# Optimization experiments

Hardware: AMD Instinct MI355X
Metric: run time of the kernel (lower is better)

Reference implementation:

```python
import jax, jax.numpy as jnp
import numpy as np
from jax.scipy.special import logsumexp

N_ITERS = 20


def setup_inputs() -> dict:
    key = jax.random.key(0)
    k1, _ = jax.random.split(key)
    cost_matrix = jax.random.uniform(k1, (64, 1024, 1024), dtype=jnp.float32)
    epsilon = jnp.ones((1,), dtype=jnp.float32)
    return {"cost_matrix": cost_matrix, "epsilon": epsilon}


def reference(cost_matrix, epsilon):
    # log-space Sinkhorn: alternate row / column normalization in log domain
    log_alpha = -cost_matrix / epsilon  # (B, N, N)

    def step(la, _):
        la = la - logsumexp(la, axis=-1, keepdims=True)  # row normalize
        la = la - logsumexp(la, axis=-2, keepdims=True)  # col normalize
        return la, None

    log_alpha, _ = jax.lax.scan(step, log_alpha, None, length=N_ITERS)
    return jnp.exp(log_alpha)
```

## Files before the change

kernel.cpp:

```cpp
#include <hip/hip_runtime.h>
#include <hip/hip_fp16.h>


#define BATCH 64
#define N 1024
#define NITERS 20
#define RPB 64
#define BPB 16
#define NBLK (BATCH * BPB)
#define THREADS 256
#define NU2 (N / 4)
#define NU4 (N / 8)
#define NU4F8 (N / 16)
#define NGRP 64
#define BAR_WORDS 128
#define PART_ELEMS ((size_t)2 * BATCH * BPB * N)
#define CSUM_FB_ELEMS ((size_t)NITERS * BATCH * N)

typedef float f32x2 __attribute__((ext_vector_type(2)));

union H2U { __half2 h; unsigned u; };

__device__ __forceinline__ float4 h4_to_f4(uint2 r) {
    H2U a, b;
    a.u = r.x; b.u = r.y;
    float2 fa = __half22float2(a.h);
    float2 fb = __half22float2(b.h);
    return make_float4(fa.x, fa.y, fb.x, fb.y);
}

__device__ __forceinline__ void h8_unpack(uint4 r, float* f) {
    H2U a, b, c, d;
    a.u = r.x; b.u = r.y; c.u = r.z; d.u = r.w;
    float2 fa = __half22float2(a.h), fb = __half22float2(b.h);
    float2 fc = __half22float2(c.h), fd = __half22float2(d.h);
    f[0] = fa.x; f[1] = fa.y; f[2] = fb.x; f[3] = fb.y;
    f[4] = fc.x; f[5] = fc.y; f[6] = fd.x; f[7] = fd.y;
}

__device__ __forceinline__ uint4 h8_pack(const float* f) {
    H2U a, b, c, d;
    a.h = __float22half2_rn(make_float2(f[0], f[1]));
    b.h = __float22half2_rn(make_float2(f[2], f[3]));
    c.h = __float22half2_rn(make_float2(f[4], f[5]));
    d.h = __float22half2_rn(make_float2(f[6], f[7]));
    uint4 r; r.x = a.u; r.y = b.u; r.z = c.u; r.w = d.u;
    return r;
}

__device__ __forceinline__ uint4 pack_fp8_16(const float* k) {
    uint4 r;
    int a;
    a = __builtin_amdgcn_cvt_pk_fp8_f32(k[0],  k[1],  0, false);
    a = __builtin_amdgcn_cvt_pk_fp8_f32(k[2],  k[3],  a, true);
    r.x = (unsigned)a;
    a = __builtin_amdgcn_cvt_pk_fp8_f32(k[4],  k[5],  0, false);
    a = __builtin_amdgcn_cvt_pk_fp8_f32(k[6],  k[7],  a, true);
    r.y = (unsigned)a;
    a = __builtin_amdgcn_cvt_pk_fp8_f32(k[8],  k[9],  0, false);
    a = __builtin_amdgcn_cvt_pk_fp8_f32(k[10], k[11], a, true);
    r.z = (unsigned)a;
    a = __builtin_amdgcn_cvt_pk_fp8_f32(k[12], k[13], 0, false);
    a = __builtin_amdgcn_cvt_pk_fp8_f32(k[14], k[15], a, true);
    r.w = (unsigned)a;
    return r;
}

__device__ __forceinline__ void unpack_fp8_16(uint4 r, float* f) {
    f32x2 p;
    p = __builtin_amdgcn_cvt_pk_f32_fp8((int)r.x, false); f[0]  = p.x; f[1]  = p.y;
    p = __builtin_amdgcn_cvt_pk_f32_fp8((int)r.x, true);  f[2]  = p.x; f[3]  = p.y;
    p = __builtin_amdgcn_cvt_pk_f32_fp8((int)r.y, false); f[4]  = p.x; f[5]  = p.y;
    p = __builtin_amdgcn_cvt_pk_f32_fp8((int)r.y, true);  f[6]  = p.x; f[7]  = p.y;
    p = __builtin_amdgcn_cvt_pk_f32_fp8((int)r.z, false); f[8]  = p.x; f[9]  = p.y;
    p = __builtin_amdgcn_cvt_pk_f32_fp8((int)r.z, true);  f[10] = p.x; f[11] = p.y;
    p = __builtin_amdgcn_cvt_pk_f32_fp8((int)r.w, false); f[12] = p.x; f[13] = p.y;
    p = __builtin_amdgcn_cvt_pk_f32_fp8((int)r.w, true);  f[14] = p.x; f[15] = p.y;
}

__device__ __forceinline__ float cload(const float* p) {
    return __hip_atomic_load((float*)p, __ATOMIC_RELAXED, __HIP_MEMORY_SCOPE_AGENT);
}
__device__ __forceinline__ void cstore(float* p, float v) {
    __hip_atomic_store(p, v, __ATOMIC_RELAXED, __HIP_MEMORY_SCOPE_AGENT);
}

__global__ __launch_bounds__(THREADS) void sk_zero(float* __restrict__ buf,
                                                   int total) {
    const int i = blockIdx.x * THREADS + threadIdx.x;
    if (i < total) buf[i] = 0.0f;
}

__device__ __forceinline__ void gbar(unsigned* __restrict__ bar,
                                     unsigned& gencount) {
    __syncthreads();
    if (threadIdx.x == 0) {
        asm volatile("" ::: "memory");
        unsigned* grp    = bar;
        unsigned* master = bar + NGRP;
        unsigned* gen    = bar + NGRP + 1;
        const unsigned gid = blockIdx.x & (NGRP - 1);
        if (__hip_atomic_fetch_add(&grp[gid], 1u, __ATOMIC_RELAXED,
                                   __HIP_MEMORY_SCOPE_AGENT) == (NBLK / NGRP) - 1u) {
            if (__hip_atomic_fetch_add(master, 1u, __ATOMIC_RELAXED,
                                       __HIP_MEMORY_SCOPE_AGENT) == NGRP - 1u) {
                #pragma unroll
                for (int i = 0; i < NGRP; ++i)
                    __hip_atomic_store(&grp[i], 0u, __ATOMIC_RELAXED,
                                       __HIP_MEMORY_SCOPE_AGENT);
                __hip_atomic_store(master, 0u, __ATOMIC_RELAXED,
                                   __HIP_MEMORY_SCOPE_AGENT);
                asm volatile("s_waitcnt vmcnt(0)" ::: "memory");
                __hip_atomic_fetch_add(gen, 1u, __ATOMIC_RELAXED,
                                       __HIP_MEMORY_SCOPE_AGENT);
            }
        }
        while (__hip_atomic_load(gen, __ATOMIC_RELAXED,
                                 __HIP_MEMORY_SCOPE_AGENT) == gencount)
            __builtin_amdgcn_s_sleep(2);
        asm volatile("" ::: "memory");
    }
    __syncthreads();
    ++gencount;
}

__global__ __launch_bounds__(THREADS, 4) void sk_fused(
        const float* __restrict__ C, const float* __restrict__ eps,
        uint4* __restrict__ K16, uint4* __restrict__ K8,
        float* __restrict__ part, unsigned* __restrict__ bar,
        float* __restrict__ out) {
    __shared__ float4 smc[4][N / 4];
    __shared__ float vsh[N];
    __shared__ float u_lds[RPB];
    const int t = threadIdx.x;
    const int lane = t & 63, w = t >> 6;
    const int bid = blockIdx.x;
    const int b = bid >> 4, bx = bid & 15;
    const int row0 = bx * RPB + w * 16;
    unsigned gencount = 0;

    {
        const float nie = -1.0f / eps[0];
        const float4* __restrict__ Cp =
            (const float4*)(C + ((size_t)b * N + row0) * N) + lane * 4;
        uint4* __restrict__ Kp16 = K16 + ((size_t)b * N + row0) * NU4 + lane * 2;
        uint4* __restrict__ Kp8  = K8  + ((size_t)b * N + row0) * NU4F8 + lane;

        float colacc[16];
        #pragma unroll
        for (int q = 0; q < 16; ++q) colacc[q] = 0.0f;

        float4 cur[4];
        #pragma unroll
        for (int q = 0; q < 4; ++q) cur[q] = Cp[q];

        #pragma unroll
        for (int i = 0; i < 16; ++i) {
            float4 nxt[4];
            if (i < 15) {
                #pragma unroll
                for (int q = 0; q < 4; ++q) nxt[q] = Cp[(i + 1) * (N / 4) + q];
            }
            float k[16];
            const float* cf = (const float*)cur;
            #pragma unroll
            for (int q = 0; q < 16; ++q) k[q] = __expf(cf[q] * nie);

            Kp16[(size_t)i * NU4]     = h8_pack(k);
            Kp16[(size_t)i * NU4 + 1] = h8_pack(k + 8);
            Kp8[(size_t)i * NU4F8]    = pack_fp8_16(k);

            float s = (((k[0] + k[1]) + (k[2] + k[3])) + ((k[4] + k[5]) + (k[6] + k[7])))
                    + (((k[8] + k[9]) + (k[10] + k[11])) + ((k[12] + k[13]) + (k[14] + k[15])));
            #pragma unroll
            for (int off = 32; off; off >>= 1) s += __shfl_xor(s, off, 64);
            const float ui = 1.0f / s;

            #pragma unroll
            for (int q = 0; q < 16; ++q) colacc[q] += k[q] * ui;

            if (i < 15) {
                #pragma unroll
                for (int q = 0; q < 4; ++q) cur[q] = nxt[q];
            }
        }

        #pragma unroll
        for (int q = 0; q < 4; ++q)
            smc[w][lane * 4 + q] = make_float4(colacc[4 * q], colacc[4 * q + 1],
                                               colacc[4 * q + 2], colacc[4 * q + 3]);
        __syncthreads();
        float4 s0 = smc[0][t], s1 = smc[1][t], s2 = smc[2][t], s3 = smc[3][t];
        float* pw = part + (((size_t)0 * BATCH + b) * BPB + bx) * N + 4 * t;
        cstore(pw + 0, (s0.x + s1.x) + (s2.x + s3.x));
        cstore(pw + 1, (s0.y + s1.y) + (s2.y + s3.y));
        cstore(pw + 2, (s0.z + s1.z) + (s2.z + s3.z));
        cstore(pw + 3, (s0.w + s1.w) + (s2.w + s3.w));
    }
    gbar(bar, gencount);

    const uint4* __restrict__ Kp8r = K8 + ((size_t)b * N + row0) * NU4F8 + lane;
    #pragma unroll 1
    for (int p = 1; p <= 18; ++p) {
        {
            const float* pb =
                part + (((size_t)((p - 1) & 1) * BATCH + b) * BPB) * N + 4 * t;
            float a0 = 0.f, a1 = 0.f, a2 = 0.f, a3 = 0.f;
            #pragma unroll
            for (int j = 0; j < BPB; ++j) {
                const float* pj = pb + (size_t)j * N;
                a0 += cload(pj + 0);
                a1 += cload(pj + 1);
                a2 += cload(pj + 2);
                a3 += cload(pj + 3);
            }
            vsh[4 * t + 0] = 1.0f / a0;
            vsh[4 * t + 1] = 1.0f / a1;
            vsh[4 * t + 2] = 1.0f / a2;
            vsh[4 * t + 3] = 1.0f / a3;
        }
        __syncthreads();
        float vv[16];
        #pragma unroll
        for (int e = 0; e < 16; ++e) vv[e] = vsh[lane * 16 + e];

        float colacc[16];
        #pragma unroll
        for (int q = 0; q < 16; ++q) colacc[q] = 0.0f;

        uint4 buf[4];
        #pragma unroll
        for (int q = 0; q < 4; ++q) buf[q] = Kp8r[(size_t)q * NU4F8];

        #pragma unroll
        for (int i = 0; i < 16; ++i) {
            uint4 nx;
            if (i < 12) nx = Kp8r[(size_t)(i + 4) * NU4F8];

            float k[16];
            unpack_fp8_16(buf[i & 3], k);

            float pa = (k[0] * vv[0] + k[1] * vv[1]) + (k[2] * vv[2] + k[3] * vv[3]);
            float pb = (k[4] * vv[4] + k[5] * vv[5]) + (k[6] * vv[6] + k[7] * vv[7]);
            float pc = (k[8] * vv[8] + k[9] * vv[9]) + (k[10] * vv[10] + k[11] * vv[11]);
            float pd = (k[12] * vv[12] + k[13] * vv[13]) + (k[14] * vv[14] + k[15] * vv[15]);
            float s = (pa + pb) + (pc + pd);

            #pragma unroll
            for (int off = 32; off; off >>= 1) s += __shfl_xor(s, off, 64);
            const float ui = 1.0f / s;

            #pragma unroll
            for (int q = 0; q < 16; ++q) colacc[q] += k[q] * ui;

            if (i < 12) buf[i & 3] = nx;
        }

        #pragma unroll
        for (int q = 0; q < 4; ++q)
            smc[w][lane * 4 + q] = make_float4(colacc[4 * q], colacc[4 * q + 1],
                                               colacc[4 * q + 2], colacc[4 * q + 3]);
        __syncthreads();
        float4 s0 = smc[0][t], s1 = smc[1][t], s2 = smc[2][t], s3 = smc[3][t];
        float* pw = part + (((size_t)(p & 1) * BATCH + b) * BPB + bx) * N + 4 * t;
        cstore(pw + 0, (s0.x + s1.x) + (s2.x + s3.x));
        cstore(pw + 1, (s0.y + s1.y) + (s2.y + s3.y));
        cstore(pw + 2, (s0.z + s1.z) + (s2.z + s3.z));
        cstore(pw + 3, (s0.w + s1.w) + (s2.w + s3.w));
        gbar(bar, gencount);
    }

    {
        {
            const float* pb = part + (((size_t)0 * BATCH + b) * BPB) * N + 4 * t;
            float a0 = 0.f, a1 = 0.f, a2 = 0.f, a3 = 0.f;
            #pragma unroll
            for (int j = 0; j < BPB; ++j) {
                const float* pj = pb + (size_t)j * N;
                a0 += cload(pj + 0);
                a1 += cload(pj + 1);
                a2 += cload(pj + 2);
                a3 += cload(pj + 3);
            }
            vsh[4 * t + 0] = 1.0f / a0;
            vsh[4 * t + 1] = 1.0f / a1;
            vsh[4 * t + 2] = 1.0f / a2;
            vsh[4 * t + 3] = 1.0f / a3;
        }
        __syncthreads();
        float vv[16];
        #pragma unroll
        for (int e = 0; e < 16; ++e) vv[e] = vsh[lane * 16 + e];

        const uint4* __restrict__ Kp = K16 + ((size_t)b * N + row0) * NU4 + lane * 2;

        float colacc[16];
        #pragma unroll
        for (int q = 0; q < 16; ++q) colacc[q] = 0.0f;

        uint4 c0 = Kp[0], c1 = Kp[1];
        #pragma unroll
        for (int i = 0; i < 16; ++i) {
            uint4 n0, n1;
            if (i < 15) {
                n0 = Kp[(size_t)(i + 1) * NU4];
                n1 = Kp[(size_t)(i + 1) * NU4 + 1];
            }
            float k[16];
            h8_unpack(c0, k);
            h8_unpack(c1, k + 8);

            float pa = (k[0] * vv[0] + k[1] * vv[1]) + (k[2] * vv[2] + k[3] * vv[3]);
            float pb = (k[4] * vv[4] + k[5] * vv[5]) + (k[6] * vv[6] + k[7] * vv[7]);
            float pc = (k[8] * vv[8] + k[9] * vv[9]) + (k[10] * vv[10] + k[11] * vv[11]);
            float pd = (k[12] * vv[12] + k[13] * vv[13]) + (k[14] * vv[14] + k[15] * vv[15]);
            float s = (pa + pb) + (pc + pd);

            #pragma unroll
            for (int off = 32; off; off >>= 1) s += __shfl_xor(s, off, 64);
            const float ui = 1.0f / s;
            if (lane == 0) u_lds[w * 16 + i] = ui;

            #pragma unroll
            for (int q = 0; q < 16; ++q) colacc[q] += k[q] * ui;

            if (i < 15) { c0 = n0; c1 = n1; }
        }

        #pragma unroll
        for (int q = 0; q < 4; ++q)
            smc[w][lane * 4 + q] = make_float4(colacc[4 * q], colacc[4 * q + 1],
                                               colacc[4 * q + 2], colacc[4 * q + 3]);
        __syncthreads();
        float4 s0 = smc[0][t], s1 = smc[1][t], s2 = smc[2][t], s3 = smc[3][t];
        float* pw = part + (((size_t)1 * BATCH + b) * BPB + bx) * N + 4 * t;
        cstore(pw + 0, (s0.x + s1.x) + (s2.x + s3.x));
        cstore(pw + 1, (s0.y + s1.y) + (s2.y + s3.y));
        cstore(pw + 2, (s0.z + s1.z) + (s2.z + s3.z));
        cstore(pw + 3, (s0.w + s1.w) + (s2.w + s3.w));
    }
    gbar(bar, gencount);

    {
        {
            const float* pb = part + (((size_t)1 * BATCH + b) * BPB) * N + 4 * t;
            float a0 = 0.f, a1 = 0.f, a2 = 0.f, a3 = 0.f;
            #pragma unroll
            for (int j = 0; j < BPB; ++j) {
                const float* pj = pb + (size_t)j * N;
                a0 += cload(pj + 0);
                a1 += cload(pj + 1);
                a2 += cload(pj + 2);
                a3 += cload(pj + 3);
            }
            vsh[4 * t + 0] = 1.0f / a0;
            vsh[4 * t + 1] = 1.0f / a1;
            vsh[4 * t + 2] = 1.0f / a2;
            vsh[4 * t + 3] = 1.0f / a3;
        }
        __syncthreads();
        const float4 vvf = make_float4(vsh[4 * t + 0], vsh[4 * t + 1],
                                       vsh[4 * t + 2], vsh[4 * t + 3]);
        const size_t rowbase = (size_t)b * N + (size_t)bx * RPB;
        const uint2* __restrict__ K2 = (const uint2*)K16;

        uint2 kc = K2[rowbase * NU2 + t];
        for (int r = 0; r < RPB; ++r) {
            uint2 kn;
            if (r < RPB - 1) kn = K2[(rowbase + r + 1) * NU2 + t];
            const float ur = u_lds[r];
            float4 k = h4_to_f4(kc);
            float4 o;
            o.x = k.x * ur * vvf.x;
            o.y = k.y * ur * vvf.y;
            o.z = k.z * ur * vvf.z;
            o.w = k.w * ur * vvf.w;
            ((float4*)(out + (rowbase + r) * N))[t] = o;
            kc = kn;
        }
    }
}


__global__ __launch_bounds__(THREADS) void sk_build(
        const float* __restrict__ C, const float* __restrict__ eps,
        uint4* __restrict__ K16, uint4* __restrict__ K8,
        float* __restrict__ u, float* __restrict__ csum_out) {
    __shared__ float4 smc[4][N / 4];
    const int t = threadIdx.x;
    const int lane = t & 63, w = t >> 6;
    const int b = blockIdx.y;
    const int row0 = blockIdx.x * RPB + w * 16;
    const float nie = -1.0f / eps[0];

    const float4* __restrict__ Cp =
        (const float4*)(C + ((size_t)b * N + row0) * N) + lane * 4;
    uint4* __restrict__ Kp16 = K16 + ((size_t)b * N + row0) * NU4 + lane * 2;
    uint4* __restrict__ Kp8  = K8  + ((size_t)b * N + row0) * NU4F8 + lane;

    float colacc[16];
    #pragma unroll
    for (int q = 0; q < 16; ++q) colacc[q] = 0.0f;

    float4 cur[4];
    #pragma unroll
    for (int q = 0; q < 4; ++q) cur[q] = Cp[q];

    for (int i = 0; i < 16; ++i) {
        float4 nxt[4];
        if (i < 15) {
            #pragma unroll
            for (int q = 0; q < 4; ++q) nxt[q] = Cp[(i + 1) * (N / 4) + q];
        }
        float k[16];
        const float* cf = (const float*)cur;
        #pragma unroll
        for (int q = 0; q < 16; ++q) k[q] = __expf(cf[q] * nie);

        Kp16[(size_t)i * NU4]     = h8_pack(k);
        Kp16[(size_t)i * NU4 + 1] = h8_pack(k + 8);
        Kp8[(size_t)i * NU4F8]    = pack_fp8_16(k);

        float s = (((k[0] + k[1]) + (k[2] + k[3])) + ((k[4] + k[5]) + (k[6] + k[7])))
                + (((k[8] + k[9]) + (k[10] + k[11])) + ((k[12] + k[13]) + (k[14] + k[15])));
        #pragma unroll
        for (int off = 32; off; off >>= 1) s += __shfl_xor(s, off, 64);
        const float ui = 1.0f / s;
        if (lane == 0) u[b * N + row0 + i] = ui;

        #pragma unroll
        for (int q = 0; q < 16; ++q) colacc[q] += k[q] * ui;

        if (i < 15) {
            #pragma unroll
            for (int q = 0; q < 4; ++q) cur[q] = nxt[q];
        }
    }

    #pragma unroll
    for (int q = 0; q < 4; ++q)
        smc[w][lane * 4 + q] = make_float4(colacc[4 * q], colacc[4 * q + 1],
                                           colacc[4 * q + 2], colacc[4 * q + 3]);
    __syncthreads();
    float4 s0 = smc[0][t], s1 = smc[1][t], s2 = smc[2][t], s3 = smc[3][t];
    float* cs = csum_out + b * N + 4 * t;
    atomicAdd(cs + 0, (s0.x + s1.x) + (s2.x + s3.x));
    atomicAdd(cs + 1, (s0.y + s1.y) + (s2.y + s3.y));
    atomicAdd(cs + 2, (s0.z + s1.z) + (s2.z + s3.z));
    atomicAdd(cs + 3, (s0.w + s1.w) + (s2.w + s3.w));
}

__global__ __launch_bounds__(THREADS) void sk_iter8(
        const uint4* __restrict__ K8, const float* __restrict__ csum_in,
        float* __restrict__ csum_out) {
    __shared__ float4 smc[4][N / 4];
    const int t = threadIdx.x;
    const int lane = t & 63, w = t >> 6;
    const int b = blockIdx.y;
    const int row0 = blockIdx.x * RPB + w * 16;

    const float4* __restrict__ cin = (const float4*)(csum_in + b * N) + lane * 4;
    float vv[16];
    #pragma unroll
    for (int q = 0; q < 4; ++q) {
        float4 c = cin[q];
        vv[4 * q + 0] = 1.0f / c.x;
        vv[4 * q + 1] = 1.0f / c.y;
        vv[4 * q + 2] = 1.0f / c.z;
        vv[4 * q + 3] = 1.0f / c.w;
    }

    const uint4* __restrict__ Kp = K8 + ((size_t)b * N + row0) * NU4F8 + lane;

    float colacc[16];
    #pragma unroll
    for (int q = 0; q < 16; ++q) colacc[q] = 0.0f;

    uint4 c0 = Kp[0];
    uint4 c1 = Kp[NU4F8];
    for (int i = 0; i < 16; ++i) {
        uint4 c2;
        if (i < 14) c2 = Kp[(size_t)(i + 2) * NU4F8];

        float k[16];
        unpack_fp8_16(c0, k);

        float pa = (k[0] * vv[0] + k[1] * vv[1]) + (k[2] * vv[2] + k[3] * vv[3]);
        float pb = (k[4] * vv[4] + k[5] * vv[5]) + (k[6] * vv[6] + k[7] * vv[7]);
        float pc = (k[8] * vv[8] + k[9] * vv[9]) + (k[10] * vv[10] + k[11] * vv[11]);
        float pd = (k[12] * vv[12] + k[13] * vv[13]) + (k[14] * vv[14] + k[15] * vv[15]);
        float s = (pa + pb) + (pc + pd);

        #pragma unroll
        for (int off = 32; off; off >>= 1) s += __shfl_xor(s, off, 64);
        const float ui = 1.0f / s;

        #pragma unroll
        for (int q = 0; q < 16; ++q) colacc[q] += k[q] * ui;

        c0 = c1;
        if (i < 14) c1 = c2;
    }

    #pragma unroll
    for (int q = 0; q < 4; ++q)
        smc[w][lane * 4 + q] = make_float4(colacc[4 * q], colacc[4 * q + 1],
                                           colacc[4 * q + 2], colacc[4 * q + 3]);
    __syncthreads();
    float4 s0 = smc[0][t], s1 = smc[1][t], s2 = smc[2][t], s3 = smc[3][t];
    float* cs = csum_out + b * N + 4 * t;
    atomicAdd(cs + 0, (s0.x + s1.x) + (s2.x + s3.x));
    atomicAdd(cs + 1, (s0.y + s1.y) + (s2.y + s3.y));
    atomicAdd(cs + 2, (s0.z + s1.z) + (s2.z + s3.z));
    atomicAdd(cs + 3, (s0.w + s1.w) + (s2.w + s3.w));
}

__global__ __launch_bounds__(THREADS) void sk_iter(
        const uint4* __restrict__ K, const float* __restrict__ csum_in,
        float* __restrict__ u, float* __restrict__ csum_out) {
    __shared__ float4 smc[4][N / 4];
    const int t = threadIdx.x;
    const int lane = t & 63, w = t >> 6;
    const int b = blockIdx.y;
    const int row0 = blockIdx.x * RPB + w * 16;

    const float4* __restrict__ cin = (const float4*)(csum_in + b * N) + lane * 4;
    float vv[16];
    #pragma unroll
    for (int q = 0; q < 4; ++q) {
        float4 c = cin[q];
        vv[4 * q + 0] = 1.0f / c.x;
        vv[4 * q + 1] = 1.0f / c.y;
        vv[4 * q + 2] = 1.0f / c.z;
        vv[4 * q + 3] = 1.0f / c.w;
    }

    const uint4* __restrict__ Kp = K + ((size_t)b * N + row0) * NU4 + lane * 2;

    float colacc[16];
    #pragma unroll
    for (int q = 0; q < 16; ++q) colacc[q] = 0.0f;

    uint4 c0 = Kp[0], c1 = Kp[1];
    for (int i = 0; i < 16; ++i) {
        uint4 n0, n1;
        if (i < 15) {
            n0 = Kp[(size_t)(i + 1) * NU4];
            n1 = Kp[(size_t)(i + 1) * NU4 + 1];
        }
        float k[16];
        h8_unpack(c0, k);
        h8_unpack(c1, k + 8);

        float pa = (k[0] * vv[0] + k[1] * vv[1]) + (k[2] * vv[2] + k[3] * vv[3]);
        float pb = (k[4] * vv[4] + k[5] * vv[5]) + (k[6] * vv[6] + k[7] * vv[7]);
        float pc = (k[8] * vv[8] + k[9] * vv[9]) + (k[10] * vv[10] + k[11] * vv[11]);
        float pd = (k[12] * vv[12] + k[13] * vv[13]) + (k[14] * vv[14] + k[15] * vv[15]);
        float s = (pa + pb) + (pc + pd);

        #pragma unroll
        for (int off = 32; off; off >>= 1) s += __shfl_xor(s, off, 64);
        const float ui = 1.0f / s;
        if (lane == 0) u[b * N + row0 + i] = ui;

        #pragma unroll
        for (int q = 0; q < 16; ++q) colacc[q] += k[q] * ui;

        if (i < 15) { c0 = n0; c1 = n1; }
    }

    #pragma unroll
    for (int q = 0; q < 4; ++q)
        smc[w][lane * 4 + q] = make_float4(colacc[4 * q], colacc[4 * q + 1],
                                           colacc[4 * q + 2], colacc[4 * q + 3]);
    __syncthreads();
    float4 s0 = smc[0][t], s1 = smc[1][t], s2 = smc[2][t], s3 = smc[3][t];
    float* cs = csum_out + b * N + 4 * t;
    atomicAdd(cs + 0, (s0.x + s1.x) + (s2.x + s3.x));
    atomicAdd(cs + 1, (s0.y + s1.y) + (s2.y + s3.y));
    atomicAdd(cs + 2, (s0.z + s1.z) + (s2.z + s3.z));
    atomicAdd(cs + 3, (s0.w + s1.w) + (s2.w + s3.w));
}

__global__ __launch_bounds__(THREADS) void sk_final(
        const uint2* __restrict__ K, const float* __restrict__ u,
        const float* __restrict__ csum_last, float* __restrict__ out) {
    const int t = threadIdx.x;
    const int row = blockIdx.x;
    const int b = blockIdx.y;
    const float ui = u[b * N + row];
    const float4 ci = ((const float4*)(csum_last + b * N))[t];
    const float4 vv = make_float4(1.0f / ci.x, 1.0f / ci.y, 1.0f / ci.z, 1.0f / ci.w);
    const size_t base = (size_t)b * N + row;
    float4 k = h4_to_f4((K + base * NU2)[t]);
    float4 o;
    o.x = k.x * ui * vv.x;
    o.y = k.y * ui * vv.y;
    o.z = k.z * ui * vv.z;
    o.w = k.w * ui * vv.w;
    ((float4*)(out + base * N))[t] = o;
}


__device__ __forceinline__ float block_reduce_broadcast(float val, float* lds) {
    #pragma unroll
    for (int off = 32; off > 0; off >>= 1)
        val += __shfl_xor(val, off, 64);
    const int lane = threadIdx.x & 63;
    const int wid  = threadIdx.x >> 6;
    if (lane == 0) lds[wid] = val;
    __syncthreads();
    float total = lds[0] + lds[1] + lds[2] + lds[3];
    __syncthreads();
    return total;
}

__global__ __launch_bounds__(THREADS) void sink_init(float* __restrict__ v,
                                                     float* __restrict__ colsum) {
    const int i = blockIdx.x * THREADS + threadIdx.x;
    v[i] = 1.0f;
    colsum[i] = 0.0f;
}

__global__ __launch_bounds__(THREADS) void sink_iter(
        const float* __restrict__ C, const float* __restrict__ eps,
        const float* __restrict__ v, float* __restrict__ u,
        float* __restrict__ colsum) {
    __shared__ float lds[4];
    const int t = threadIdx.x;
    const int b = blockIdx.y;
    const int row0 = blockIdx.x * RPB;
    const float neg_inv_eps = -1.0f / eps[0];

    const float4 vv = ((const float4*)(v + b * N))[t];
    const float4* __restrict__ Cp = (const float4*)(C + ((size_t)b * N + row0) * N);

    float4 colacc = make_float4(0.f, 0.f, 0.f, 0.f);
    float4 cur = Cp[t];
    for (int i = 0; i < RPB; ++i) {
        float4 nxt = cur;
        if (i + 1 < RPB)
            nxt = Cp[(size_t)(i + 1) * (N / 4) + t];

        float4 k;
        k.x = __expf(cur.x * neg_inv_eps);
        k.y = __expf(cur.y * neg_inv_eps);
        k.z = __expf(cur.z * neg_inv_eps);
        k.w = __expf(cur.w * neg_inv_eps);

        float s = k.x * vv.x + k.y * vv.y + k.z * vv.z + k.w * vv.w;
        float S = block_reduce_broadcast(s, lds);
        float ui = 1.0f / S;
        if (t == 0) u[b * N + row0 + i] = ui;

        colacc.x += k.x * ui;
        colacc.y += k.y * ui;
        colacc.z += k.z * ui;
        colacc.w += k.w * ui;
        cur = nxt;
    }

    float* cs = colsum + b * N + 4 * t;
    atomicAdd(cs + 0, colacc.x);
    atomicAdd(cs + 1, colacc.y);
    atomicAdd(cs + 2, colacc.z);
    atomicAdd(cs + 3, colacc.w);
}

__global__ __launch_bounds__(THREADS) void sink_fix(float* __restrict__ v,
                                                    float* __restrict__ colsum) {
    const int i = blockIdx.x * THREADS + threadIdx.x;
    v[i] = 1.0f / colsum[i];
    colsum[i] = 0.0f;
}

__global__ __launch_bounds__(THREADS) void sink_final(
        const float* __restrict__ C, const float* __restrict__ eps,
        const float* __restrict__ u, const float* __restrict__ v,
        float* __restrict__ out) {
    const int t = threadIdx.x;
    const int row = blockIdx.x;
    const int b = blockIdx.y;
    const float neg_inv_eps = -1.0f / eps[0];
    const float ui = u[b * N + row];
    const float4 vv = ((const float4*)(v + b * N))[t];
    const size_t base = ((size_t)b * N + row) * N;
    float4 c = ((const float4*)(C + base))[t];
    float4 o;
    o.x = __expf(c.x * neg_inv_eps) * ui * vv.x;
    o.y = __expf(c.y * neg_inv_eps) * ui * vv.y;
    o.z = __expf(c.z * neg_inv_eps) * ui * vv.z;
    o.w = __expf(c.w * neg_inv_eps) * ui * vv.w;
    ((float4*)(out + base))[t] = o;
}


extern "C" void kernel_launch(void* const* d_in, const int* in_sizes, int n_in,
                              void* d_out, int out_size, void* d_ws, size_t ws_size,
                              hipStream_t stream) {
    const float* C   = (const float*)d_in[0];
    const float* eps = (const float*)d_in[1];
    float* out = (float*)d_out;

    const size_t k16_bytes  = (size_t)BATCH * N * N * 2;
    const size_t k8_bytes   = (size_t)BATCH * N * N;
    const size_t part_bytes = PART_ELEMS * 4;
    const size_t uv_elems   = (size_t)BATCH * N;
    const size_t needed     = k16_bytes + k8_bytes + part_bytes +
                              BAR_WORDS * 4 + uv_elems * 4 + CSUM_FB_ELEMS * 4;

    if (ws_size >= needed) {
        uint4* K16    = (uint4*)d_ws;
        uint4* K8     = (uint4*)((char*)d_ws + k16_bytes);
        float* part   = (float*)((char*)d_ws + k16_bytes + k8_bytes);
        unsigned* bar = (unsigned*)(part + PART_ELEMS);
        float* u      = (float*)(bar + BAR_WORDS);
        float* csum   = u + uv_elems;

        static int coop_ok = -1;
        if (coop_ok < 0) {
            int nb = 0;
            hipError_t e = hipOccupancyMaxActiveBlocksPerMultiprocessor(
                &nb, sk_fused, THREADS, 0);
            coop_ok = (e == hipSuccess && nb >= 4) ? 1 : 0;
        }

        if (coop_ok) {
            sk_zero<<<dim3(1), dim3(THREADS), 0, stream>>>((float*)bar, BAR_WORDS);
            sk_fused<<<dim3(NBLK), dim3(THREADS), 0, stream>>>(
                C, eps, K16, K8, part, bar, out);
        } else {
            const int zero_total = (int)CSUM_FB_ELEMS;
            sk_zero<<<dim3((zero_total + THREADS - 1) / THREADS), dim3(THREADS),
                      0, stream>>>(csum, zero_total);
            sk_build<<<dim3(BPB, BATCH), dim3(THREADS), 0, stream>>>(
                C, eps, K16, K8, u, csum);
            for (int it = 2; it <= NITERS - 1; ++it) {
                sk_iter8<<<dim3(BPB, BATCH), dim3(THREADS), 0, stream>>>(
                    K8, csum + (size_t)(it - 2) * uv_elems,
                    csum + (size_t)(it - 1) * uv_elems);
            }
            sk_iter<<<dim3(BPB, BATCH), dim3(THREADS), 0, stream>>>(
                K16, csum + (size_t)(NITERS - 2) * uv_elems, u,
                csum + (size_t)(NITERS - 1) * uv_elems);
            sk_final<<<dim3(N, BATCH), dim3(THREADS), 0, stream>>>(
                (const uint2*)K16, u, csum + (size_t)(NITERS - 1) * uv_elems, out);
        }
    } else {
        float* u      = (float*)d_ws;
        float* v      = u + uv_elems;
        float* colsum = v + uv_elems;
        sink_init<<<dim3(BATCH * N / THREADS), dim3(THREADS), 0, stream>>>(v, colsum);
        for (int it = 0; it < NITERS; ++it) {
            sink_iter<<<dim3(BPB, BATCH), dim3(THREADS), 0, stream>>>(
                C, eps, v, u, colsum);
            sink_fix<<<dim3(BATCH * N / THREADS), dim3(THREADS), 0, stream>>>(v, colsum);
        }
        sink_final<<<dim3(N, BATCH), dim3(THREADS), 0, stream>>>(C, eps, u, v, out);
    }
}
```

Before: 1.019 ms.

## Replace grid-wide barrier with per-batch reducer-block column-sum exchange

The global barrier across all 1024 blocks is replaced by a per-batch barrier over the 16 blocks that share a batch. The last-arriving block reduces the partial column sums, computes the inverse column scales, and publishes them to a global v buffer. The other blocks wait on a per-batch generation counter and then read v, which removes the redundant 16-way partial reduction each block used to do. The v staging in shared memory is padded to a stride of 17 to avoid bank conflicts. In exchange, a single reducer block sits on the critical path, and the partial buffer is no longer double-buffered, which depends on the barrier ordering being correct.

```diff
diff --git a/kernel.cpp b/kernel.cpp
--- a/kernel.cpp
+++ b/kernel.cpp
@@ -12,9 +12,11 @@
 #define NU2 (N / 4)
 #define NU4 (N / 8)
 #define NU4F8 (N / 16)
-#define NGRP 64
-#define BAR_WORDS 128
-#define PART_ELEMS ((size_t)2 * BATCH * BPB * N)
+#define VSH_STRIDE 17
+#define BAR_STRIDE 32
+#define PART_ELEMS ((size_t)BATCH * BPB * N)
+#define VBUF_ELEMS ((size_t)BATCH * N)
+#define BAR_WORDS (BATCH * BAR_STRIDE)
 #define CSUM_FB_ELEMS ((size_t)NITERS * BATCH * N)
 
 typedef float f32x2 __attribute__((ext_vector_type(2)));
@@ -84,6 +86,9 @@
 __device__ __forceinline__ void cstore(float* p, float v) {
     __hip_atomic_store(p, v, __ATOMIC_RELAXED, __HIP_MEMORY_SCOPE_AGENT);
 }
+__device__ __forceinline__ unsigned cloadu(const unsigned* p) {
+    return __hip_atomic_load((unsigned*)p, __ATOMIC_RELAXED, __HIP_MEMORY_SCOPE_AGENT);
+}
 
 __global__ __launch_bounds__(THREADS) void sk_zero(float* __restrict__ buf,
                                                    int total) {
@@ -91,52 +96,89 @@
     if (i < total) buf[i] = 0.0f;
 }
 
-__device__ __forceinline__ void gbar(unsigned* __restrict__ bar,
-                                     unsigned& gencount) {
-    __syncthreads();
-    if (threadIdx.x == 0) {
-        asm volatile("" ::: "memory");
-        unsigned* grp    = bar;
-        unsigned* master = bar + NGRP;
-        unsigned* gen    = bar + NGRP + 1;
-        const unsigned gid = blockIdx.x & (NGRP - 1);
-        if (__hip_atomic_fetch_add(&grp[gid], 1u, __ATOMIC_RELAXED,
-                                   __HIP_MEMORY_SCOPE_AGENT) == (NBLK / NGRP) - 1u) {
-            if (__hip_atomic_fetch_add(master, 1u, __ATOMIC_RELAXED,
-                                       __HIP_MEMORY_SCOPE_AGENT) == NGRP - 1u) {
-                #pragma unroll
-                for (int i = 0; i < NGRP; ++i)
-                    __hip_atomic_store(&grp[i], 0u, __ATOMIC_RELAXED,
-                                       __HIP_MEMORY_SCOPE_AGENT);
-                __hip_atomic_store(master, 0u, __ATOMIC_RELAXED,
+__device__ __forceinline__ void colsum_exchange(
+        float4 ps, float* __restrict__ partb, float* __restrict__ vb,
+        unsigned* __restrict__ arrive, unsigned* __restrict__ gen,
+        unsigned& gencount, float* __restrict__ vshp,
+        unsigned* __restrict__ redf, int t, int bx) {
+    float* pw = partb + (size_t)bx * N + 4 * t;
+    cstore(pw + 0, ps.x);
+    cstore(pw + 1, ps.y);
+    cstore(pw + 2, ps.z);
+    cstore(pw + 3, ps.w);
+    __syncthreads();
+    if (t == 0) {
+        *redf = (__hip_atomic_fetch_add(arrive, 1u, __ATOMIC_RELAXED,
+                                        __HIP_MEMORY_SCOPE_AGENT) == BPB - 1u)
+                    ? 1u : 0u;
+    }
+    __syncthreads();
+    const bool reducer = (*redf != 0u);
+    const int c0 = 4 * t;
+    const int vbase = (c0 >> 4) * VSH_STRIDE + (c0 & 15);
+    if (reducer) {
+        float a0 = 0.f, a1 = 0.f, a2 = 0.f, a3 = 0.f;
+        const float* pr = partb + c0;
+        #pragma unroll
+        for (int j = 0; j < BPB; ++j) {
+            const float* pj = pr + (size_t)j * N;
+            a0 += cload(pj + 0);
+            a1 += cload(pj + 1);
+            a2 += cload(pj + 2);
+            a3 += cload(pj + 3);
+        }
+        const float i0 = 1.0f / a0, i1 = 1.0f / a1;
+        const float i2 = 1.0f / a2, i3 = 1.0f / a3;
+        cstore(vb + c0 + 0, i0);
+        cstore(vb + c0 + 1, i1);
+        cstore(vb + c0 + 2, i2);
+        cstore(vb + c0 + 3, i3);
+        vshp[vbase + 0] = i0;
+        vshp[vbase + 1] = i1;
+        vshp[vbase + 2] = i2;
+        vshp[vbase + 3] = i3;
+        __syncthreads();
+        if (t == 0) {
+            __hip_atomic_store(arrive, 0u, __ATOMIC_RELAXED,
+                               __HIP_MEMORY_SCOPE_AGENT);
+            asm volatile("s_waitcnt vmcnt(0)" ::: "memory");
+            __hip_atomic_fetch_add(gen, 1u, __ATOMIC_RELAXED,
                                    __HIP_MEMORY_SCOPE_AGENT);
-                asm volatile("s_waitcnt vmcnt(0)" ::: "memory");
-                __hip_atomic_fetch_add(gen, 1u, __ATOMIC_RELAXED,
-                                       __HIP_MEMORY_SCOPE_AGENT);
-            }
-        }
-        while (__hip_atomic_load(gen, __ATOMIC_RELAXED,
-                                 __HIP_MEMORY_SCOPE_AGENT) == gencount)
+        }
+    }
+    if (t == 0) {
+        while (cloadu(gen) == gencount)
             __builtin_amdgcn_s_sleep(2);
-        asm volatile("" ::: "memory");
     }
     __syncthreads();
     ++gencount;
+    if (!reducer) {
+        vshp[vbase + 0] = cload(vb + c0 + 0);
+        vshp[vbase + 1] = cload(vb + c0 + 1);
+        vshp[vbase + 2] = cload(vb + c0 + 2);
+        vshp[vbase + 3] = cload(vb + c0 + 3);
+    }
+    __syncthreads();
 }
 
 __global__ __launch_bounds__(THREADS, 4) void sk_fused(
         const float* __restrict__ C, const float* __restrict__ eps,
         uint4* __restrict__ K16, uint4* __restrict__ K8,
-        float* __restrict__ part, unsigned* __restrict__ bar,
-        float* __restrict__ out) {
+        float* __restrict__ part, float* __restrict__ vbuf,
+        unsigned* __restrict__ bar, float* __restrict__ out) {
     __shared__ float4 smc[4][N / 4];
-    __shared__ float vsh[N];
+    __shared__ float vshp[64 * VSH_STRIDE];
     __shared__ float u_lds[RPB];
+    __shared__ unsigned redf;
     const int t = threadIdx.x;
     const int lane = t & 63, w = t >> 6;
     const int bid = blockIdx.x;
     const int b = bid >> 4, bx = bid & 15;
     const int row0 = bx * RPB + w * 16;
+    unsigned* arrive = bar + b * BAR_STRIDE;
+    unsigned* gen    = arrive + 1;
+    float* partb = part + (size_t)b * BPB * N;
+    float* vb    = vbuf + (size_t)b * N;
     unsigned gencount = 0;
 
     {
@@ -191,38 +233,20 @@
                                                colacc[4 * q + 2], colacc[4 * q + 3]);
         __syncthreads();
         float4 s0 = smc[0][t], s1 = smc[1][t], s2 = smc[2][t], s3 = smc[3][t];
-        float* pw = part + (((size_t)0 * BATCH + b) * BPB + bx) * N + 4 * t;
-        cstore(pw + 0, (s0.x + s1.x) + (s2.x + s3.x));
-        cstore(pw + 1, (s0.y + s1.y) + (s2.y + s3.y));
-        cstore(pw + 2, (s0.z + s1.z) + (s2.z + s3.z));
-        cstore(pw + 3, (s0.w + s1.w) + (s2.w + s3.w));
-    }
-    gbar(bar, gencount);
+        float4 ps;
+        ps.x = (s0.x + s1.x) + (s2.x + s3.x);
+        ps.y = (s0.y + s1.y) + (s2.y + s3.y);
+        ps.z = (s0.z + s1.z) + (s2.z + s3.z);
+        ps.w = (s0.w + s1.w) + (s2.w + s3.w);
+        colsum_exchange(ps, partb, vb, arrive, gen, gencount, vshp, &redf, t, bx);
+    }
 
     const uint4* __restrict__ Kp8r = K8 + ((size_t)b * N + row0) * NU4F8 + lane;
     #pragma unroll 1
     for (int p = 1; p <= 18; ++p) {
-        {
-            const float* pb =
-                part + (((size_t)((p - 1) & 1) * BATCH + b) * BPB) * N + 4 * t;
-            float a0 = 0.f, a1 = 0.f, a2 = 0.f, a3 = 0.f;
-            #pragma unroll
-            for (int j = 0; j < BPB; ++j) {
-                const float* pj = pb + (size_t)j * N;
-                a0 += cload(pj + 0);
-                a1 += cload(pj + 1);
-                a2 += cload(pj + 2);
-                a3 += cload(pj + 3);
-            }
-            vsh[4 * t + 0] = 1.0f / a0;
-            vsh[4 * t + 1] = 1.0f / a1;
-            vsh[4 * t + 2] = 1.0f / a2;
-            vsh[4 * t + 3] = 1.0f / a3;
-        }
-        __syncthreads();
         float vv[16];
         #pragma unroll
-        for (int e = 0; e < 16; ++e) vv[e] = vsh[lane * 16 + e];
+        for (int e = 0; e < 16; ++e) vv[e] = vshp[lane * VSH_STRIDE + e];
 
         float colacc[16];
         #pragma unroll
@@ -262,35 +286,18 @@
                                                colacc[4 * q + 2], colacc[4 * q + 3]);
         __syncthreads();
         float4 s0 = smc[0][t], s1 = smc[1][t], s2 = smc[2][t], s3 = smc[3][t];
-        float* pw = part + (((size_t)(p & 1) * BATCH + b) * BPB + bx) * N + 4 * t;
-        cstore(pw + 0, (s0.x + s1.x) + (s2.x + s3.x));
-        cstore(pw + 1, (s0.y + s1.y) + (s2.y + s3.y));
-        cstore(pw + 2, (s0.z + s1.z) + (s2.z + s3.z));
-        cstore(pw + 3, (s0.w + s1.w) + (s2.w + s3.w));
-        gbar(bar, gencount);
+        float4 ps;
+        ps.x = (s0.x + s1.x) + (s2.x + s3.x);
+        ps.y = (s0.y + s1.y) + (s2.y + s3.y);
+        ps.z = (s0.z + s1.z) + (s2.z + s3.z);
+        ps.w = (s0.w + s1.w) + (s2.w + s3.w);
+        colsum_exchange(ps, partb, vb, arrive, gen, gencount, vshp, &redf, t, bx);
     }
 
     {
-        {
-            const float* pb = part + (((size_t)0 * BATCH + b) * BPB) * N + 4 * t;
-            float a0 = 0.f, a1 = 0.f, a2 = 0.f, a3 = 0.f;
-            #pragma unroll
-            for (int j = 0; j < BPB; ++j) {
-                const float* pj = pb + (size_t)j * N;
-                a0 += cload(pj + 0);
-                a1 += cload(pj + 1);
-                a2 += cload(pj + 2);
-                a3 += cload(pj + 3);
-            }
-            vsh[4 * t + 0] = 1.0f / a0;
-            vsh[4 * t + 1] = 1.0f / a1;
-            vsh[4 * t + 2] = 1.0f / a2;
-            vsh[4 * t + 3] = 1.0f / a3;
-        }
-        __syncthreads();
         float vv[16];
         #pragma unroll
-        for (int e = 0; e < 16; ++e) vv[e] = vsh[lane * 16 + e];
+        for (int e = 0; e < 16; ++e) vv[e] = vshp[lane * VSH_STRIDE + e];
 
         const uint4* __restrict__ Kp = K16 + ((size_t)b * N + row0) * NU4 + lane * 2;
 
@@ -333,34 +340,19 @@
                                                colacc[4 * q + 2], colacc[4 * q + 3]);
         __syncthreads();
         float4 s0 = smc[0][t], s1 = smc[1][t], s2 = smc[2][t], s3 = smc[3][t];
-        float* pw = part + (((size_t)1 * BATCH + b) * BPB + bx) * N + 4 * t;
-        cstore(pw + 0, (s0.x + s1.x) + (s2.x + s3.x));
-        cstore(pw + 1, (s0.y + s1.y) + (s2.y + s3.y));
-        cstore(pw + 2, (s0.z + s1.z) + (s2.z + s3.z));
-        cstore(pw + 3, (s0.w + s1.w) + (s2.w + s3.w));
-    }
-    gbar(bar, gencount);
+        float4 ps;
+        ps.x = (s0.x + s1.x) + (s2.x + s3.x);
+        ps.y = (s0.y + s1.y) + (s2.y + s3.y);
+        ps.z = (s0.z + s1.z) + (s2.z + s3.z);
+        ps.w = (s0.w + s1.w) + (s2.w + s3.w);
+        colsum_exchange(ps, partb, vb, arrive, gen, gencount, vshp, &redf, t, bx);
+    }
 
     {
-        {
-            const float* pb = part + (((size_t)1 * BATCH + b) * BPB) * N + 4 * t;
-            float a0 = 0.f, a1 = 0.f, a2 = 0.f, a3 = 0.f;
-            #pragma unroll
-            for (int j = 0; j < BPB; ++j) {
-                const float* pj = pb + (size_t)j * N;
-                a0 += cload(pj + 0);
-                a1 += cload(pj + 1);
-                a2 += cload(pj + 2);
-                a3 += cload(pj + 3);
-            }
-            vsh[4 * t + 0] = 1.0f / a0;
-            vsh[4 * t + 1] = 1.0f / a1;
-            vsh[4 * t + 2] = 1.0f / a2;
-            vsh[4 * t + 3] = 1.0f / a3;
-        }
-        __syncthreads();
-        const float4 vvf = make_float4(vsh[4 * t + 0], vsh[4 * t + 1],
-                                       vsh[4 * t + 2], vsh[4 * t + 3]);
+        const int c0 = 4 * t;
+        const int vbase = (c0 >> 4) * VSH_STRIDE + (c0 & 15);
+        const float4 vvf = make_float4(vshp[vbase + 0], vshp[vbase + 1],
+                                       vshp[vbase + 2], vshp[vbase + 3]);
         const size_t rowbase = (size_t)b * N + (size_t)bx * RPB;
         const uint2* __restrict__ K2 = (const uint2*)K16;
 
@@ -705,15 +697,18 @@
     const size_t k16_bytes  = (size_t)BATCH * N * N * 2;
     const size_t k8_bytes   = (size_t)BATCH * N * N;
     const size_t part_bytes = PART_ELEMS * 4;
+    const size_t vbuf_bytes = VBUF_ELEMS * 4;
+    const size_t bar_bytes  = BAR_WORDS * 4;
     const size_t uv_elems   = (size_t)BATCH * N;
-    const size_t needed     = k16_bytes + k8_bytes + part_bytes +
-                              BAR_WORDS * 4 + uv_elems * 4 + CSUM_FB_ELEMS * 4;
+    const size_t needed     = k16_bytes + k8_bytes + part_bytes + vbuf_bytes +
+                              bar_bytes + uv_elems * 4 + CSUM_FB_ELEMS * 4;
 
     if (ws_size >= needed) {
         uint4* K16    = (uint4*)d_ws;
         uint4* K8     = (uint4*)((char*)d_ws + k16_bytes);
         float* part   = (float*)((char*)d_ws + k16_bytes + k8_bytes);
-        unsigned* bar = (unsigned*)(part + PART_ELEMS);
+        float* vbuf   = part + PART_ELEMS;
+        unsigned* bar = (unsigned*)(vbuf + VBUF_ELEMS);
         float* u      = (float*)(bar + BAR_WORDS);
         float* csum   = u + uv_elems;
 
@@ -726,9 +721,10 @@
         }
 
         if (coop_ok) {
-            sk_zero<<<dim3(1), dim3(THREADS), 0, stream>>>((float*)bar, BAR_WORDS);
+            sk_zero<<<dim3((BAR_WORDS + THREADS - 1) / THREADS), dim3(THREADS),
+                      0, stream>>>((float*)bar, BAR_WORDS);
             sk_fused<<<dim3(NBLK), dim3(THREADS), 0, stream>>>(
-                C, eps, K16, K8, part, bar, out);
+                C, eps, K16, K8, part, vbuf, bar, out);
         } else {
             const int zero_total = (int)CSUM_FB_ELEMS;
             sk_zero<<<dim3((zero_total + THREADS - 1) / THREADS), dim3(THREADS),
```

Result: no change. 1.010 ms (-0.8%).
